# Kernel tuning notes

Hardware: AMD Instinct MI355X
Metric: run time of the kernel (lower is better)

## Reference

```python
import jax, jax.numpy as jnp
import numpy as np

H = 64  # hidden_dim
D = 16  # input_dim


def _gru_scan(x, w_ih, w_hh, b_ih, b_hh):
    """Single-direction GRU (PyTorch gate order r,z,n).
    x: [B,T,D] -> ys: [T,B,H] (hidden at each step), h_last: [B,H]."""
    B = x.shape[0]
    # precompute input-to-gate projections for all timesteps: [T,B,3H]
    xg = jnp.einsum('btd,gd->tbg', x, w_ih) + b_ih
    h0 = jnp.zeros((B, w_hh.shape[1]), dtype=x.dtype)

    def step(h, xg_t):
        hg = h @ w_hh.T + b_hh                      # [B,3H]
        xr, xz, xn = jnp.split(xg_t, 3, axis=-1)
        hr, hz, hn = jnp.split(hg, 3, axis=-1)
        r = jax.nn.sigmoid(xr + hr)
        z = jax.nn.sigmoid(xz + hz)
        n = jnp.tanh(xn + r * hn)
        h_new = (1.0 - z) * n + z * h
        return h_new, h_new

    h_last, ys = jax.lax.scan(step, h0, xg)
    return ys, h_last


def setup_inputs() -> dict:
    key = jax.random.key(0)
    ks = jax.random.split(key, 11)
    B, T = 512, 512
    s_i = 1.0 / np.sqrt(H)
    x = jax.random.normal(ks[0], (B, T, D), dtype=jnp.float32)
    def u(k, shape):
        return jax.random.uniform(k, shape, dtype=jnp.float32, minval=-s_i, maxval=s_i)
    return {
        'x': x,
        'w_ih_f': u(ks[1], (3 * H, D)), 'w_hh_f': u(ks[2], (3 * H, H)),
        'b_ih_f': u(ks[3], (3 * H,)),  'b_hh_f': u(ks[4], (3 * H,)),
        'w_ih_b': u(ks[5], (3 * H, D)), 'w_hh_b': u(ks[6], (3 * H, H)),
        'b_ih_b': u(ks[7], (3 * H,)),  'b_hh_b': u(ks[8], (3 * H,)),
        'fc_w': u(ks[9], (1, 2 * H)),  'fc_b': u(ks[10], (1,)),
    }


def reference(x, w_ih_f, w_hh_f, b_ih_f, b_hh_f,
              w_ih_b, w_hh_b, b_ih_b, b_hh_b, fc_w, fc_b):
    # forward direction: output at t=T-1 is the final carry
    _, h_fwd_last = _gru_scan(x, w_ih_f, w_hh_f, b_ih_f, b_hh_f)
    # backward direction: runs over reversed time; its output at original
    # t=T-1 is the FIRST step of the reversed scan
    ys_b, _ = _gru_scan(x[:, ::-1, :], w_ih_b, w_hh_b, b_ih_b, b_hh_b)
    h_bwd_at_last = ys_b[0]                          # [B,H]
    out_last = jnp.concatenate([h_fwd_last, h_bwd_at_last], axis=-1)  # [B,2H]
    y = out_last @ fc_w.T + fc_b                     # [B,1]
    return jnp.squeeze(y, axis=-1)                   # [B]
```

## Files before the change

kernel.cpp:

```cpp
#include <hip/hip_runtime.h>


#define Hh 64
#define Dd 16
#define Tt 512
#define Bb 512
#define CH 16
#define NC (Tt / CH)
#define BUFSZ (CH * Hh)

typedef _Float16 half2v __attribute__((ext_vector_type(2)));

__device__ __forceinline__ float rcp_fast(float v) { return __builtin_amdgcn_rcpf(v); }
__device__ __forceinline__ float sigmoid_fast(float v) {
    return rcp_fast(1.0f + __expf(-v));
}
__device__ __forceinline__ float tanh_fast(float v) {
    return 1.0f - 2.0f * rcp_fast(__expf(2.0f * v) + 1.0f);
}
__device__ __forceinline__ float dot4(float4 a, float4 b) {
    return a.x * b.x + a.y * b.y + a.z * b.z + a.w * b.w;
}
__device__ __forceinline__ float fd2(half2v a, half2v b, float c) {
    return __builtin_amdgcn_fdot2(a, b, c, false);
}
__device__ __forceinline__ half2v bc_h2(float f) {
    union { float f; half2v h; } u; u.f = f; return u.h;
}
__device__ __forceinline__ void lds_barrier() {
    asm volatile("s_waitcnt lgkmcnt(0)\n\ts_barrier" ::: "memory");
}

#define DUO(U, P)                                                            \
    {                                                                        \
        const half2v p0_ = bc_h2(U.x), p1_ = bc_h2(U.y);                     \
        const half2v p2_ = bc_h2(U.z), p3_ = bc_h2(U.w);                     \
        sr0 = fd2(wrh[4*(P)+0], p0_, sr0);                                   \
        sz0 = fd2(wzh[4*(P)+0], p0_, sz0);                                   \
        sn0 = fd2(wnh[4*(P)+0], p0_, sn0);                                   \
        sr1 = fd2(wrh[4*(P)+1], p1_, sr1);                                   \
        sz1 = fd2(wzh[4*(P)+1], p1_, sz1);                                   \
        sn1 = fd2(wnh[4*(P)+1], p1_, sn1);                                   \
        sr0 = fd2(wrh[4*(P)+2], p2_, sr0);                                   \
        sz0 = fd2(wzh[4*(P)+2], p2_, sz0);                                   \
        sn0 = fd2(wnh[4*(P)+2], p2_, sn0);                                   \
        sr1 = fd2(wrh[4*(P)+3], p3_, sr1);                                   \
        sz1 = fd2(wzh[4*(P)+3], p3_, sz1);                                   \
        sn1 = fd2(wnh[4*(P)+3], p3_, sn1);                                   \
    }

__global__ __launch_bounds__(256, 2)
void bigru_pc_kernel(const float* __restrict__ x,
                     const float* __restrict__ w_ih_f, const float* __restrict__ w_hh_f,
                     const float* __restrict__ b_ih_f, const float* __restrict__ b_hh_f,
                     const float* __restrict__ w_ih_b, const float* __restrict__ w_hh_b,
                     const float* __restrict__ b_ih_b, const float* __restrict__ b_hh_b,
                     const float* __restrict__ fc_w,  const float* __restrict__ fc_b,
                     float* __restrict__ out)
{
    const int tid  = threadIdx.x;
    const int j    = tid & 63;
    const int w    = tid >> 6;
    const int b    = blockIdx.x;
    const int cons = b & 3;

    __shared__ __align__(16) float4    xgs4[2 * BUFSZ];
    __shared__ __align__(16) _Float16  hbuf16[Hh];

    const float* xrow = x + (size_t)b * Tt * Dd;

    if (w == cons) {
        half2v wrh[Hh/2], wzh[Hh/2], wnh[Hh/2];
        {
            const float4* r0 = (const float4*)(w_hh_f + (size_t)j            * Hh);
            const float4* r1 = (const float4*)(w_hh_f + (size_t)(Hh + j)     * Hh);
            const float4* r2 = (const float4*)(w_hh_f + (size_t)(2 * Hh + j) * Hh);
#pragma unroll
            for (int q = 0; q < Hh / 4; ++q) {
                float4 a = r0[q];
                wrh[2*q]   = (half2v){(_Float16)a.x, (_Float16)a.y};
                wrh[2*q+1] = (half2v){(_Float16)a.z, (_Float16)a.w};
                float4 c = r1[q];
                wzh[2*q]   = (half2v){(_Float16)c.x, (_Float16)c.y};
                wzh[2*q+1] = (half2v){(_Float16)c.z, (_Float16)c.w};
                float4 e = r2[q];
                wnh[2*q]   = (half2v){(_Float16)e.x, (_Float16)e.y};
                wnh[2*q+1] = (half2v){(_Float16)e.z, (_Float16)e.w};
            }
        }
        const float bhnr = b_hh_f[2 * Hh + j];
        float h = 0.0f;

        for (int c = 0; c < NC; ++c) {
            lds_barrier();
            const float4* base = xgs4 + (c & 1) * BUFSZ + j;
            float4 pg = base[0];
#pragma unroll 2
            for (int t = 0; t < CH; ++t) {
                hbuf16[j] = (_Float16)h;
                const float4* hq = (const float4*)hbuf16;
                float4 u0 = hq[0], u1 = hq[1], u2 = hq[2], u3 = hq[3];
                float4 u4 = hq[4], u5 = hq[5], u6 = hq[6], u7 = hq[7];
                float4 ng = base[((t + 1) & (CH - 1)) * Hh];

                float sr0 = 0.f, sr1 = 0.f, sz0 = 0.f, sz1 = 0.f;
                float sn0 = 0.f, sn1 = 0.f;
                DUO(u0, 0) DUO(u1, 1) DUO(u2, 2) DUO(u3, 3)
                DUO(u4, 4) DUO(u5, 5) DUO(u6, 6) DUO(u7, 7)

                const float r = sigmoid_fast(pg.x + (sr0 + sr1));
                const float z = sigmoid_fast(pg.y + (sz0 + sz1));
                const float n = tanh_fast(pg.z + r * (bhnr + (sn0 + sn1)));
                h = n + z * (h - n);
                pg = ng;
            }
        }

        float ar   = b_ih_b[j]          + b_hh_b[j];
        float az   = b_ih_b[Hh + j]     + b_hh_b[Hh + j];
        float axn  = b_ih_b[2 * Hh + j];
        const float bhnb = b_hh_b[2 * Hh + j];
        {
            const float4* xl = (const float4*)(xrow + (size_t)(Tt - 1) * Dd);
            float4 xv0 = xl[0], xv1 = xl[1], xv2 = xl[2], xv3 = xl[3];
            const float4* q0 = (const float4*)(w_ih_b + (size_t)j            * Dd);
            const float4* q1 = (const float4*)(w_ih_b + (size_t)(Hh + j)     * Dd);
            const float4* q2 = (const float4*)(w_ih_b + (size_t)(2 * Hh + j) * Dd);
            ar  += dot4(q0[0], xv0) + dot4(q0[1], xv1) + dot4(q0[2], xv2) + dot4(q0[3], xv3);
            az  += dot4(q1[0], xv0) + dot4(q1[1], xv1) + dot4(q1[2], xv2) + dot4(q1[3], xv3);
            axn += dot4(q2[0], xv0) + dot4(q2[1], xv1) + dot4(q2[2], xv2) + dot4(q2[3], xv3);
        }
        const float rb = sigmoid_fast(ar);
        const float zb = sigmoid_fast(az);
        const float nb = tanh_fast(axn + rb * bhnb);
        const float hb = (1.0f - zb) * nb;

        float v = fc_w[j] * h + fc_w[Hh + j] * hb;
#pragma unroll
        for (int off = 32; off > 0; off >>= 1)
            v += __shfl_xor(v, off, 64);
        if (j == 0) out[b] = v + fc_b[0];
    } else {
        const int pw = (w > cons) ? (w - 1) : w;
        float4 wir[4], wiz[4], win[4];
        {
            const float4* p0 = (const float4*)(w_ih_f + (size_t)j            * Dd);
            const float4* p1 = (const float4*)(w_ih_f + (size_t)(Hh + j)     * Dd);
            const float4* p2 = (const float4*)(w_ih_f + (size_t)(2 * Hh + j) * Dd);
#pragma unroll
            for (int q = 0; q < 4; ++q) { wir[q] = p0[q]; wiz[q] = p1[q]; win[q] = p2[q]; }
        }
        const float bxr = b_ih_f[j]          + b_hh_f[j];
        const float bxz = b_ih_f[Hh + j]     + b_hh_f[Hh + j];
        const float bxn = b_ih_f[2 * Hh + j];

#define PRODUCE(C1) {                                                        \
            float4* obase = xgs4 + ((C1) & 1) * BUFSZ + j;                   \
            for (int tt = pw; tt < CH; tt += 3) {                            \
                const float4* xq = (const float4*)(xrow + (size_t)((C1) * CH + tt) * Dd); \
                float4 x0 = xq[0], x1 = xq[1], x2 = xq[2], x3 = xq[3];       \
                float ar_ = bxr + dot4(wir[0],x0) + dot4(wir[1],x1)          \
                                + dot4(wir[2],x2) + dot4(wir[3],x3);         \
                float az_ = bxz + dot4(wiz[0],x0) + dot4(wiz[1],x1)          \
                                + dot4(wiz[2],x2) + dot4(wiz[3],x3);         \
                float an_ = bxn + dot4(win[0],x0) + dot4(win[1],x1)          \
                                + dot4(win[2],x2) + dot4(win[3],x3);         \
                obase[tt * Hh] = make_float4(ar_, az_, an_, 0.0f);           \
            }                                                                \
        }

        PRODUCE(0);
        for (int c = 0; c < NC; ++c) {
            lds_barrier();
            if (c + 1 < NC) PRODUCE(c + 1);
        }
#undef PRODUCE
    }
}

extern "C" void kernel_launch(void* const* d_in, const int* in_sizes, int n_in,
                              void* d_out, int out_size, void* d_ws, size_t ws_size,
                              hipStream_t stream) {
    const float* x      = (const float*)d_in[0];
    const float* w_ih_f = (const float*)d_in[1];
    const float* w_hh_f = (const float*)d_in[2];
    const float* b_ih_f = (const float*)d_in[3];
    const float* b_hh_f = (const float*)d_in[4];
    const float* w_ih_b = (const float*)d_in[5];
    const float* w_hh_b = (const float*)d_in[6];
    const float* b_ih_b = (const float*)d_in[7];
    const float* b_hh_b = (const float*)d_in[8];
    const float* fc_w   = (const float*)d_in[9];
    const float* fc_b   = (const float*)d_in[10];

    bigru_pc_kernel<<<dim3(Bb), dim3(256), 0, stream>>>(
        x, w_ih_f, w_hh_f, b_ih_f, b_hh_f,
        w_ih_b, w_hh_b, b_ih_b, b_hh_b, fc_w, fc_b,
        (float*)d_out);
}
```

Before: 269.2 us.

## Accumulate r/z gate dot products with packed f16 FMA, unroll chunk fully

The r and z recurrent dot products now accumulate in packed half2 registers with v_pk_fma_f16 instead of fdot2 into f32, and are reduced to float only at the end. The n gate keeps f32 fdot2 accumulation. The 16-step chunk loop is fully unrolled, and the consumer wave raises its scheduling priority with s_setprio. This is meant to shorten the serial per-step latency of the recurrence, at the cost of lower accumulation precision for the r and z gates.

```diff
diff --git a/kernel.cpp b/kernel.cpp
--- a/kernel.cpp
+++ b/kernel.cpp
@@ -24,6 +24,9 @@
 __device__ __forceinline__ float fd2(half2v a, half2v b, float c) {
     return __builtin_amdgcn_fdot2(a, b, c, false);
 }
+__device__ __forceinline__ void pkfma16(half2v& a, half2v b, half2v c) {
+    asm("v_pk_fma_f16 %0, %1, %2, %0" : "+v"(a) : "v"(b), "v"(c));
+}
 __device__ __forceinline__ half2v bc_h2(float f) {
     union { float f; half2v h; } u; u.f = f; return u.h;
 }
@@ -31,23 +34,45 @@
     asm volatile("s_waitcnt lgkmcnt(0)\n\ts_barrier" ::: "memory");
 }
 
-#define DUO(U, P)                                                            \
+#define MIX(U, P)                                                            \
     {                                                                        \
         const half2v p0_ = bc_h2(U.x), p1_ = bc_h2(U.y);                     \
         const half2v p2_ = bc_h2(U.z), p3_ = bc_h2(U.w);                     \
-        sr0 = fd2(wrh[4*(P)+0], p0_, sr0);                                   \
-        sz0 = fd2(wzh[4*(P)+0], p0_, sz0);                                   \
+        pkfma16(ra0, wrh[4*(P)+0], p0_);                                     \
+        pkfma16(za0, wzh[4*(P)+0], p0_);                                     \
         sn0 = fd2(wnh[4*(P)+0], p0_, sn0);                                   \
-        sr1 = fd2(wrh[4*(P)+1], p1_, sr1);                                   \
-        sz1 = fd2(wzh[4*(P)+1], p1_, sz1);                                   \
+        pkfma16(ra1, wrh[4*(P)+1], p1_);                                     \
+        pkfma16(za1, wzh[4*(P)+1], p1_);                                     \
         sn1 = fd2(wnh[4*(P)+1], p1_, sn1);                                   \
-        sr0 = fd2(wrh[4*(P)+2], p2_, sr0);                                   \
-        sz0 = fd2(wzh[4*(P)+2], p2_, sz0);                                   \
+        pkfma16(ra0, wrh[4*(P)+2], p2_);                                     \
+        pkfma16(za0, wzh[4*(P)+2], p2_);                                     \
         sn0 = fd2(wnh[4*(P)+2], p2_, sn0);                                   \
-        sr1 = fd2(wrh[4*(P)+3], p3_, sr1);                                   \
-        sz1 = fd2(wzh[4*(P)+3], p3_, sz1);                                   \
+        pkfma16(ra1, wrh[4*(P)+3], p3_);                                     \
+        pkfma16(za1, wzh[4*(P)+3], p3_);                                     \
         sn1 = fd2(wnh[4*(P)+3], p3_, sn1);                                   \
     }
+
+#define STEPT(T) do {                                                        \
+    hbuf16[j] = (_Float16)h;               \
+    const float4* hq = (const float4*)hbuf16;        \
+    float4 u0 = hq[0], u1 = hq[1], u2 = hq[2], u3 = hq[3];                   \
+    float4 u4 = hq[4], u5 = hq[5], u6 = hq[6], u7 = hq[7];                   \
+    const float4 ng = base[(((T) + 1) & (CH - 1)) * Hh];                     \
+    half2v ra0 = {0,0}, ra1 = {0,0}, za0 = {0,0}, za1 = {0,0};               \
+    float sn0 = 0.f, sn1 = 0.f;                                              \
+    MIX(u0, 0) MIX(u1, 1) MIX(u2, 2) MIX(u3, 3)                              \
+    MIX(u4, 4) MIX(u5, 5) MIX(u6, 6) MIX(u7, 7)                              \
+    const half2v rs = ra0 + ra1;                                             \
+    const half2v zs = za0 + za1;                                             \
+    const float sr = (float)rs.x + (float)rs.y;                              \
+    const float sz = (float)zs.x + (float)zs.y;                              \
+    const float sn = sn0 + sn1;                                              \
+    const float r = sigmoid_fast(pg.x + sr);                                 \
+    const float z = sigmoid_fast(pg.y + sz);                                 \
+    const float n = tanh_fast(pg.z + r * (bhnr + sn));                       \
+    h = n + z * (h - n);                                                     \
+    pg = ng;                                                                 \
+} while (0)
 
 __global__ __launch_bounds__(256, 2)
 void bigru_pc_kernel(const float* __restrict__ x,
@@ -70,6 +95,7 @@
     const float* xrow = x + (size_t)b * Tt * Dd;
 
     if (w == cons) {
+        __builtin_amdgcn_s_setprio(1);
         half2v wrh[Hh/2], wzh[Hh/2], wnh[Hh/2];
         {
             const float4* r0 = (const float4*)(w_hh_f + (size_t)j            * Hh);
@@ -95,25 +121,10 @@
             lds_barrier();
             const float4* base = xgs4 + (c & 1) * BUFSZ + j;
             float4 pg = base[0];
-#pragma unroll 2
-            for (int t = 0; t < CH; ++t) {
-                hbuf16[j] = (_Float16)h;
-                const float4* hq = (const float4*)hbuf16;
-                float4 u0 = hq[0], u1 = hq[1], u2 = hq[2], u3 = hq[3];
-                float4 u4 = hq[4], u5 = hq[5], u6 = hq[6], u7 = hq[7];
-                float4 ng = base[((t + 1) & (CH - 1)) * Hh];
-
-                float sr0 = 0.f, sr1 = 0.f, sz0 = 0.f, sz1 = 0.f;
-                float sn0 = 0.f, sn1 = 0.f;
-                DUO(u0, 0) DUO(u1, 1) DUO(u2, 2) DUO(u3, 3)
-                DUO(u4, 4) DUO(u5, 5) DUO(u6, 6) DUO(u7, 7)
-
-                const float r = sigmoid_fast(pg.x + (sr0 + sr1));
-                const float z = sigmoid_fast(pg.y + (sz0 + sz1));
-                const float n = tanh_fast(pg.z + r * (bhnr + (sn0 + sn1)));
-                h = n + z * (h - n);
-                pg = ng;
-            }
+            STEPT(0);  STEPT(1);  STEPT(2);  STEPT(3);
+            STEPT(4);  STEPT(5);  STEPT(6);  STEPT(7);
+            STEPT(8);  STEPT(9);  STEPT(10); STEPT(11);
+            STEPT(12); STEPT(13); STEPT(14); STEPT(15);
         }
 
         float ar   = b_ih_b[j]          + b_hh_b[j];
```

After: 245.8 us. 1.1x faster.
